# Performance work log

Measured on AMD Instinct MI355X. Metric: run time of the kernel, lower is better.

## Reference

```python
import jax, jax.numpy as jnp
import numpy as np

# SSD prior config (small VGGLite-style)
FEATURE_MAPS = [10, 5, 3, 1]
BOXES_PER_LOC = [4, 4, 4, 4]
IMG = 128      # ssd_config.DATA.SHAPE[0] -> WhereTransformer image_size
OBJ = 64
ZWHAT = 64
HID = 512
B = 4
N_OBJ = sum(f * f for f in FEATURE_MAPS)                       # 135
N_FEAT = sum(b * f * f for f, b in zip(FEATURE_MAPS, BOXES_PER_LOC))  # 540


def reconstruction_indices():
    # Replicates Decoder.reconstruction_indices: map per-location latents to per-box slots.
    idx = []
    last = 0
    for f, bpl in zip(FEATURE_MAPS, BOXES_PER_LOC):
        for i in range(f * f):
            idx.extend([last + i] * bpl)
        last += f * f
    return np.asarray(idx, dtype=np.int32)


def what_decode(z, W1, b1, W2, b2):
    # WhatDecoder: MLP z_what -> 3xOBJxOBJ object glyph in (0,1)
    h = jax.nn.relu(z @ W1 + b1)
    return jax.nn.sigmoid(h @ W2 + b2).reshape(-1, 3, OBJ, OBJ)


def where_stn(imgs, zw):
    # WhereTransformer: paste each object image into its (cx, cy, w, h) box on an IMGxIMG canvas
    # via inverse-affine bilinear sampling with zero padding (STN / grid_sample semantics).
    cx, cy, w, h = zw[:, 0], zw[:, 1], zw[:, 2], zw[:, 3]
    w = jnp.maximum(w, 1e-2)
    h = jnp.maximum(h, 1e-2)
    lin = jnp.linspace(-1.0, 1.0, IMG)
    gy, gx = jnp.meshgrid(lin, lin, indexing='ij')           # (IMG, IMG)
    u = (gx[None] - (2.0 * cx - 1.0)[:, None, None]) / w[:, None, None]
    v = (gy[None] - (2.0 * cy - 1.0)[:, None, None]) / h[:, None, None]
    px = (u + 1.0) * 0.5 * (OBJ - 1)                          # (N, IMG, IMG)
    py = (v + 1.0) * 0.5 * (OBJ - 1)

    def sample_one(img, py, px):  # img: (3, OBJ, OBJ)
        x0 = jnp.floor(px); y0 = jnp.floor(py)
        wx = px - x0; wy = py - y0
        x0i = x0.astype(jnp.int32); y0i = y0.astype(jnp.int32)

        def tap(yi, xi, wgt):
            valid = (yi >= 0) & (yi < OBJ) & (xi >= 0) & (xi < OBJ)
            yc = jnp.clip(yi, 0, OBJ - 1)
            xc = jnp.clip(xi, 0, OBJ - 1)
            return img[:, yc, xc] * (wgt * valid)[None]

        return (tap(y0i, x0i, (1 - wy) * (1 - wx)) + tap(y0i, x0i + 1, (1 - wy) * wx)
                + tap(y0i + 1, x0i, wy * (1 - wx)) + tap(y0i + 1, x0i + 1, wy * wx))

    return jax.vmap(sample_one)(imgs, py, px)                 # (N, 3, IMG, IMG)


def setup_inputs() -> dict:
    key = jax.random.key(0)
    ks = jax.random.split(key, 8)
    return {
        'z_what': jax.random.normal(ks[0], (B, N_OBJ, ZWHAT), jnp.float32),
        'z_where': jax.random.uniform(ks[1], (B, N_FEAT, 4), jnp.float32),
        'z_depth': jax.random.normal(ks[2], (B, N_OBJ, 1), jnp.float32),
        'W1': jax.random.normal(ks[3], (ZWHAT, HID), jnp.float32) * 0.05,
        'b1': jnp.zeros((HID,), jnp.float32),
        'W2': jax.random.normal(ks[4], (HID, 3 * OBJ * OBJ), jnp.float32) * 0.02,
        'b2': jnp.zeros((3 * OBJ * OBJ,), jnp.float32),
        'z_present': jax.random.randint(ks[5], (B, N_FEAT, 1), 0, 2, jnp.int32),
    }


def reference(z_what, z_where, z_depth, W1, b1, W2, b2, z_present):
    idx = jnp.asarray(reconstruction_indices())
    # index_select: replicate per-location latents across boxes-per-location
    zw_full = z_what[:, idx]                                  # (B, N_FEAT, ZWHAT)
    zd_full = z_depth[:, idx]                                 # (B, N_FEAT, 1)
    # sort descending by depth; gather all latents in that order
    order = jnp.argsort(-zd_full[..., 0], axis=1)             # (B, N_FEAT)
    s_what = jnp.take_along_axis(zw_full, order[..., None], axis=1)
    s_where = jnp.take_along_axis(z_where, order[..., None], axis=1)
    s_pres = jnp.take_along_axis(z_present, order[..., None], axis=1)
    # decode + STN warp all objects; absent objects are zeroed (equivalent to the
    dec = what_decode(s_what.reshape(-1, ZWHAT), W1, b1, W2, b2)
    warped = where_stn(dec, s_where.reshape(-1, 4))
    imgs = warped.reshape(B, N_FEAT, 3, IMG, IMG) * s_pres.astype(warped.dtype)[..., None, None]
    # depth compositing: per channel-pixel, take the first nonzero value in sorted order
    nz = imgs != 0
    first = jnp.argmax(nz, axis=1)                            # (B, 3, IMG, IMG)
    out = jnp.take_along_axis(imgs, first[:, None], axis=1)[:, 0] * nz.any(axis=1)
    return out
```

## Files before the change

### kernel.cpp

```cpp
#include <hip/hip_runtime.h>
#include <hip/hip_bf16.h>
#include <math.h>

#define NBOX  540
#define NOBJ  135
#define ZW    64
#define HIDN  512
#define NOUT  12288
#define OBJS  64
#define BATCH 4
#define MROWS 540
#define MPAD  640

#define PRE_SORT   4
#define PRE_GEMM1  MPAD
#define PRE_CVT    ((NOUT / 64) * (HIDN / 64))
#define PRE_BLOCKS (PRE_SORT + PRE_GEMM1 + PRE_CVT)

#define OFF_N      0u
#define OFF_PARAMS 256u
#define OFF_OBJS   34816u
#define OFF_HBF    43520u
#define OFF_W2T    698880u
#define OFF_DEC    13281792u

typedef short  bf16x8 __attribute__((ext_vector_type(8)));
typedef float  f32x4  __attribute__((ext_vector_type(4)));

#define GLOAD_LDS16(gp, lp)                                                    \
  __builtin_amdgcn_global_load_lds(                                            \
      (const __attribute__((address_space(1))) void*)(gp),                     \
      (__attribute__((address_space(3))) void*)(lp), 16, 0, 0)

__device__ __forceinline__ unsigned short f2bf(float x) {
  __hip_bfloat16 h = __float2bfloat16(x);
  return *(unsigned short*)&h;
}

__global__ __launch_bounds__(256) void k_pre(
    const float* __restrict__ z_depth,
    const float* __restrict__ z_where,
    const int*   __restrict__ z_present,
    const float* __restrict__ Z,
    const float* __restrict__ W1,
    const float* __restrict__ b1,
    const float* __restrict__ W2,
    float4* __restrict__ params,
    int*    __restrict__ objs,
    int*    __restrict__ n_present,
    unsigned short* __restrict__ Hbf,
    unsigned short* __restrict__ W2T)
{
  __shared__ unsigned long long keys[256];
  __shared__ int wsums[4], woff[4];
  __shared__ float zs[ZW];
  __shared__ unsigned int T[64 * 36];

  const int bid = blockIdx.x;
  const int t   = threadIdx.x;

  if (bid < PRE_SORT) {
    const int b = bid;
    unsigned long long key = ~0ull;
    if (t < NOBJ) {
      unsigned u = __float_as_uint(z_depth[b * NOBJ + t]);
      u = (u & 0x80000000u) ? ~u : (u | 0x80000000u);
      key = ((unsigned long long)(~u) << 32) | (unsigned)t;
    }
    keys[t] = key;
    __syncthreads();
    for (int k = 2; k <= 256; k <<= 1) {
      for (int j = k >> 1; j > 0; j >>= 1) {
        int ixj = t ^ j;
        if (ixj > t) {
          unsigned long long a = keys[t], c = keys[ixj];
          bool asc = (t & k) == 0;
          if (asc ? (a > c) : (a < c)) { keys[t] = c; keys[ixj] = a; }
        }
        __syncthreads();
      }
    }
    int boxq[3]; int presq[3]; int cnt = 0;
#pragma unroll
    for (int q = 0; q < 3; q++) {
      int e = 3 * t + q;
      presq[q] = 0; boxq[q] = 0;
      if (e < NBOX) {
        int o  = (int)(keys[e >> 2] & 0xFFFFFFFFull);
        int bx = o * 4 + (e & 3);
        boxq[q]  = bx;
        presq[q] = (z_present[b * NBOX + bx] != 0) ? 1 : 0;
        cnt += presq[q];
      }
    }
    int lane = t & 63, wv = t >> 6;
    int incl = cnt;
#pragma unroll
    for (int o = 1; o < 64; o <<= 1) {
      int vprev = __shfl_up(incl, o, 64);
      if (lane >= o) incl += vprev;
    }
    if (lane == 63) wsums[wv] = incl;
    __syncthreads();
    if (t == 0) {
      int a = 0;
#pragma unroll
      for (int i = 0; i < 4; i++) { woff[i] = a; a += wsums[i]; }
      n_present[b] = a;
    }
    __syncthreads();
    int slot = woff[wv] + incl - cnt;
#pragma unroll
    for (int q = 0; q < 3; q++) {
      if (presq[q]) {
        const float* zw = z_where + ((size_t)b * NBOX + boxq[q]) * 4;
        params[b * NBOX + slot] = make_float4(zw[0], zw[1], zw[2], zw[3]);
        objs[b * NBOX + slot]   = boxq[q] >> 2;
        slot++;
      }
    }
  } else if (bid < PRE_SORT + PRE_GEMM1) {
    const int r = bid - PRE_SORT;
    if (r >= MROWS) {
      Hbf[(size_t)r * HIDN + t] = 0;
      Hbf[(size_t)r * HIDN + t + 256] = 0;
      return;
    }
    if (t < ZW) zs[t] = Z[(size_t)r * ZW + t];
    __syncthreads();
    float a0 = b1[t], a1 = b1[t + 256];
#pragma unroll 8
    for (int k = 0; k < ZW; k++) {
      float z = zs[k];
      a0 += z * W1[(size_t)k * HIDN + t];
      a1 += z * W1[(size_t)k * HIDN + t + 256];
    }
    Hbf[(size_t)r * HIDN + t]       = f2bf(fmaxf(a0, 0.f));
    Hbf[(size_t)r * HIDN + t + 256] = f2bf(fmaxf(a1, 0.f));
  } else {
    const int c  = bid - PRE_SORT - PRE_GEMM1;
    const int n0 = (c % (NOUT / 64)) * 64;
    const int k0 = (c / (NOUT / 64)) * 64;
#pragma unroll
    for (int p = 0; p < 2; p++) {
      int kp = p * 16 + (t >> 4);
      int n4 = t & 15;
      int k  = k0 + kp * 2;
      float4 a = *(const float4*)&W2[(size_t)k * NOUT + n0 + n4 * 4];
      float4 b = *(const float4*)&W2[(size_t)(k + 1) * NOUT + n0 + n4 * 4];
      T[(n4*4 + 0) * 36 + kp] = (unsigned)f2bf(a.x) | ((unsigned)f2bf(b.x) << 16);
      T[(n4*4 + 1) * 36 + kp] = (unsigned)f2bf(a.y) | ((unsigned)f2bf(b.y) << 16);
      T[(n4*4 + 2) * 36 + kp] = (unsigned)f2bf(a.z) | ((unsigned)f2bf(b.z) << 16);
      T[(n4*4 + 3) * 36 + kp] = (unsigned)f2bf(a.w) | ((unsigned)f2bf(b.w) << 16);
    }
    __syncthreads();
#pragma unroll
    for (int p = 0; p < 2; p++) {
      int cc = p * 256 + t;
      int n = cc >> 3, ch = cc & 7;
      uint4 v = *(const uint4*)&T[n * 36 + ch * 4];
      *(uint4*)&W2T[(size_t)(n0 + n) * HIDN + k0 + ch * 8] = v;
    }
  }
}

__global__ __launch_bounds__(256) void k_gemm2_mfma(
    const unsigned short* __restrict__ Hbf,
    const unsigned short* __restrict__ W2T,
    const float* __restrict__ b2,
    float* __restrict__ dec)
{
  __shared__ unsigned short As[128 * 32];
  __shared__ unsigned short Bs[128 * 32];
  const int t    = threadIdx.x;
  const int lane = t & 63, wv = t >> 6;
  const int n0 = blockIdx.x * 128;
  const int m0 = blockIdx.y * 128;
  const int wm = (wv & 1) * 64, wn = (wv >> 1) * 64;

  const int r0 = t >> 2;
  const int kc0 = (t & 3) ^ (r0 & 3);
  const int r1 = r0 + 64;
  const int kc1 = (t & 3) ^ (r1 & 3);

  const int fr = lane & 15;
  const int fj = lane >> 4;
  f32x4 acc[4][4] = {};

  for (int k0 = 0; k0 < HIDN; k0 += 32) {
    GLOAD_LDS16(Hbf + (size_t)(m0 + r0) * HIDN + k0 + kc0 * 8, &As[t * 8]);
    GLOAD_LDS16(Hbf + (size_t)(m0 + r1) * HIDN + k0 + kc1 * 8, &As[(t + 256) * 8]);
    GLOAD_LDS16(W2T + (size_t)(n0 + r0) * HIDN + k0 + kc0 * 8, &Bs[t * 8]);
    GLOAD_LDS16(W2T + (size_t)(n0 + r1) * HIDN + k0 + kc1 * 8, &Bs[(t + 256) * 8]);
    __syncthreads();

    bf16x8 av[4], bv[4];
#pragma unroll
    for (int mi = 0; mi < 4; mi++) {
      int row = wm + mi * 16 + fr;
      av[mi] = *(const bf16x8*)&As[(row * 4 + (fj ^ (row & 3))) * 8];
    }
#pragma unroll
    for (int ni = 0; ni < 4; ni++) {
      int row = wn + ni * 16 + fr;
      bv[ni] = *(const bf16x8*)&Bs[(row * 4 + (fj ^ (row & 3))) * 8];
    }
#pragma unroll
    for (int mi = 0; mi < 4; mi++)
#pragma unroll
      for (int ni = 0; ni < 4; ni++)
        acc[mi][ni] = __builtin_amdgcn_mfma_f32_16x16x32_bf16(av[mi], bv[ni], acc[mi][ni], 0, 0, 0);
    __syncthreads();
  }

#pragma unroll
  for (int ni = 0; ni < 4; ni++) {
    int col = n0 + wn + ni * 16 + fr;
    float bb = b2[col];
#pragma unroll
    for (int mi = 0; mi < 4; mi++) {
#pragma unroll
      for (int r = 0; r < 4; r++) {
        int row = m0 + wm + mi * 16 + fj * 4 + r;
        if (row < MROWS) {
          float v = acc[mi][ni][r] + bb;
          dec[(size_t)row * NOUT + col] = 1.0f / (1.0f + __expf(-v));
        }
      }
    }
  }
}

__global__ __launch_bounds__(256) void k_composite(
    const float4* __restrict__ params, const int* __restrict__ objs,
    const int* __restrict__ n_present, const float* __restrict__ dec,
    float* __restrict__ out)
{
#pragma clang fp contract(off)
  __shared__ float4 sp[NBOX];
  __shared__ int sobj[NBOX];
  const int gid = blockIdx.x * 256 + threadIdx.x;
  const int b   = gid >> 14;
  const int pix = gid & 16383;
  const int y = pix >> 7, x = pix & 127;
  const int n = n_present[b];
  for (int i = threadIdx.x; i < n; i += 256) {
    sp[i]   = params[b * NBOX + i];
    sobj[i] = objs[b * NBOX + i];
  }
  __syncthreads();

  const double step = 2.0 / 127.0;
  const double gx = (x == 127) ? 1.0 : ((double)x * step + (-1.0));
  const double gy = (y == 127) ? 1.0 : ((double)y * step + (-1.0));

  float o0 = 0.f, o1 = 0.f, o2 = 0.f;
  bool done = false;
  for (int j = 0; j < n; j++) {
    if (__all((int)done)) break;
    if (!done) {
      float4 p = sp[j];
      double w = fmax((double)p.z, 0.01);
      double h = fmax((double)p.w, 0.01);
      double tx = 2.0 * (double)p.x - 1.0;
      double ty = 2.0 * (double)p.y - 1.0;
      double u = (gx - tx) / w;
      double v = (gy - ty) / h;
      double px = (u + 1.0) * 0.5 * 63.0;
      double py = (v + 1.0) * 0.5 * 63.0;
      double fx = floor(px), fy = floor(py);
      double wx = px - fx, wy = py - fy;
      int x0 = (int)fx, y0 = (int)fy;
      int x1 = x0 + 1, y1 = y0 + 1;
      bool vx0 = (x0 >= 0) && (x0 < OBJS);
      bool vx1 = (x1 >= 0) && (x1 < OBJS);
      bool vy0 = (y0 >= 0) && (y0 < OBJS);
      bool vy1 = (y1 >= 0) && (y1 < OBJS);
      double w00 = (1.0 - wy) * (1.0 - wx);
      double w01 = (1.0 - wy) * wx;
      double w10 = wy * (1.0 - wx);
      double w11 = wy * wx;
      bool c00 = vy0 && vx0 && (w00 > 0.0);
      bool c01 = vy0 && vx1 && (w01 > 0.0);
      bool c10 = vy1 && vx0 && (w10 > 0.0);
      bool c11 = vy1 && vx1 && (w11 > 0.0);
      if (c00 | c01 | c10 | c11) {
        const float* g = dec + (size_t)(b * NOBJ + sobj[j]) * NOUT;
        double s0 = 0.0, s1 = 0.0, s2 = 0.0;
        if (c00) { int o = y0*64 + x0; s0 += g[o]*w00; s1 += g[4096+o]*w00; s2 += g[8192+o]*w00; }
        if (c01) { int o = y0*64 + x1; s0 += g[o]*w01; s1 += g[4096+o]*w01; s2 += g[8192+o]*w01; }
        if (c10) { int o = y1*64 + x0; s0 += g[o]*w10; s1 += g[4096+o]*w10; s2 += g[8192+o]*w10; }
        if (c11) { int o = y1*64 + x1; s0 += g[o]*w11; s1 += g[4096+o]*w11; s2 += g[8192+o]*w11; }
        o0 = (float)s0; o1 = (float)s1; o2 = (float)s2;
        done = true;
      }
    }
  }
  const int ob = b * 3 * 16384 + pix;
  out[ob]         = o0;
  out[ob + 16384] = o1;
  out[ob + 32768] = o2;
}

extern "C" void kernel_launch(void* const* d_in, const int* in_sizes, int n_in,
                              void* d_out, int out_size, void* d_ws, size_t ws_size,
                              hipStream_t stream) {
  (void)in_sizes; (void)n_in; (void)out_size; (void)ws_size;
  const float* z_what    = (const float*)d_in[0];
  const float* z_where   = (const float*)d_in[1];
  const float* z_depth   = (const float*)d_in[2];
  const float* W1        = (const float*)d_in[3];
  const float* b1        = (const float*)d_in[4];
  const float* W2        = (const float*)d_in[5];
  const float* b2        = (const float*)d_in[6];
  const int*   z_present = (const int*)d_in[7];
  float* out = (float*)d_out;
  char* ws = (char*)d_ws;

  int*            n_present = (int*)(ws + OFF_N);
  float4*         params    = (float4*)(ws + OFF_PARAMS);
  int*            objs      = (int*)(ws + OFF_OBJS);
  unsigned short* Hbf       = (unsigned short*)(ws + OFF_HBF);
  unsigned short* W2T       = (unsigned short*)(ws + OFF_W2T);
  float*          dec       = (float*)(ws + OFF_DEC);

  k_pre<<<dim3(PRE_BLOCKS), dim3(256), 0, stream>>>(
      z_depth, z_where, z_present, z_what, W1, b1, W2,
      params, objs, n_present, Hbf, W2T);
  k_gemm2_mfma<<<dim3(NOUT / 128, MPAD / 128), dim3(256), 0, stream>>>(Hbf, W2T, b2, dec);
  k_composite<<<dim3(256), dim3(256), 0, stream>>>(params, objs, n_present, dec, out);
}
```

Before: 140.4 us.

## Fuse pre, GEMM and composite into one cooperative persistent kernel

Merges the three launches (prep/sort/GEMM1/W2 convert, MFMA GEMM2, compositing) into a single cooperative kernel of 480 blocks separated by grid-wide syncs, reusing one LDS buffer across phases. The compositing phase now maps each block to a 16x16 pixel tile instead of a row strip, aiming for better spatial coherence in the early-exit loop. This removes launch gaps but adds two grid barriers and serializes the formerly parallel prep work over fewer blocks.

```diff
diff --git a/kernel.cpp b/kernel.cpp
--- a/kernel.cpp
+++ b/kernel.cpp
@@ -1,6 +1,9 @@
 #include <hip/hip_runtime.h>
+#include <hip/hip_cooperative_groups.h>
 #include <hip/hip_bf16.h>
 #include <math.h>
+
+namespace cg = cooperative_groups;
 
 #define NBOX  540
 #define NOBJ  135
@@ -11,11 +14,8 @@
 #define BATCH 4
 #define MROWS 540
 #define MPAD  640
-
-#define PRE_SORT   4
-#define PRE_GEMM1  MPAD
-#define PRE_CVT    ((NOUT / 64) * (HIDN / 64))
-#define PRE_BLOCKS (PRE_SORT + PRE_GEMM1 + PRE_CVT)
+#define GRID  480
+#define CVTJOBS ((NOUT / 64) * (HIDN / 64))
 
 #define OFF_N      0u
 #define OFF_PARAMS 256u
@@ -37,7 +37,7 @@
   return *(unsigned short*)&h;
 }
 
-__global__ __launch_bounds__(256) void k_pre(
+__global__ __launch_bounds__(256, 2) void k_fused(
     const float* __restrict__ z_depth,
     const float* __restrict__ z_where,
     const int*   __restrict__ z_present,
@@ -45,22 +45,75 @@
     const float* __restrict__ W1,
     const float* __restrict__ b1,
     const float* __restrict__ W2,
+    const float* __restrict__ b2,
     float4* __restrict__ params,
     int*    __restrict__ objs,
     int*    __restrict__ n_present,
     unsigned short* __restrict__ Hbf,
-    unsigned short* __restrict__ W2T)
+    unsigned short* __restrict__ W2T,
+    float* __restrict__ dec,
+    float* __restrict__ out)
 {
-  __shared__ unsigned long long keys[256];
+  __shared__ __align__(16) unsigned char lds_raw[16384];
   __shared__ int wsums[4], woff[4];
-  __shared__ float zs[ZW];
-  __shared__ unsigned int T[64 * 36];
-
   const int bid = blockIdx.x;
   const int t   = threadIdx.x;
-
-  if (bid < PRE_SORT) {
-    const int b = bid;
+  cg::grid_group grid = cg::this_grid();
+
+  {
+    float* zs = (float*)lds_raw;
+    for (int r = bid; r < MPAD; r += GRID) {
+      if (r >= MROWS) {
+        Hbf[(size_t)r * HIDN + t] = 0;
+        Hbf[(size_t)r * HIDN + t + 256] = 0;
+      } else {
+        __syncthreads();
+        if (t < ZW) zs[t] = Z[(size_t)r * ZW + t];
+        __syncthreads();
+        float a0 = b1[t], a1 = b1[t + 256];
+#pragma unroll 8
+        for (int k = 0; k < ZW; k++) {
+          float z = zs[k];
+          a0 += z * W1[(size_t)k * HIDN + t];
+          a1 += z * W1[(size_t)k * HIDN + t + 256];
+        }
+        Hbf[(size_t)r * HIDN + t]       = f2bf(fmaxf(a0, 0.f));
+        Hbf[(size_t)r * HIDN + t + 256] = f2bf(fmaxf(a1, 0.f));
+      }
+    }
+  }
+  {
+    unsigned int* T = (unsigned int*)lds_raw;
+    for (int j = bid; j < CVTJOBS; j += GRID) {
+      __syncthreads();
+      const int n0 = (j % (NOUT / 64)) * 64;
+      const int k0 = (j / (NOUT / 64)) * 64;
+#pragma unroll
+      for (int p = 0; p < 2; p++) {
+        int kp = p * 16 + (t >> 4);
+        int n4 = t & 15;
+        int k  = k0 + kp * 2;
+        float4 a = *(const float4*)&W2[(size_t)k * NOUT + n0 + n4 * 4];
+        float4 b = *(const float4*)&W2[(size_t)(k + 1) * NOUT + n0 + n4 * 4];
+        T[(n4*4 + 0) * 36 + kp] = (unsigned)f2bf(a.x) | ((unsigned)f2bf(b.x) << 16);
+        T[(n4*4 + 1) * 36 + kp] = (unsigned)f2bf(a.y) | ((unsigned)f2bf(b.y) << 16);
+        T[(n4*4 + 2) * 36 + kp] = (unsigned)f2bf(a.z) | ((unsigned)f2bf(b.z) << 16);
+        T[(n4*4 + 3) * 36 + kp] = (unsigned)f2bf(a.w) | ((unsigned)f2bf(b.w) << 16);
+      }
+      __syncthreads();
+#pragma unroll
+      for (int p = 0; p < 2; p++) {
+        int cc = p * 256 + t;
+        int n = cc >> 3, ch = cc & 7;
+        uint4 v = *(const uint4*)&T[n * 36 + ch * 4];
+        *(uint4*)&W2T[(size_t)(n0 + n) * HIDN + k0 + ch * 8] = v;
+      }
+    }
+  }
+  if (bid >= GRID - 4) {
+    const int b = bid - (GRID - 4);
+    unsigned long long* keys = (unsigned long long*)lds_raw;
+    __syncthreads();
     unsigned long long key = ~0ull;
     if (t < NOBJ) {
       unsigned u = __float_as_uint(z_depth[b * NOBJ + t]);
@@ -119,187 +172,141 @@
         slot++;
       }
     }
-  } else if (bid < PRE_SORT + PRE_GEMM1) {
-    const int r = bid - PRE_SORT;
-    if (r >= MROWS) {
-      Hbf[(size_t)r * HIDN + t] = 0;
-      Hbf[(size_t)r * HIDN + t + 256] = 0;
-      return;
-    }
-    if (t < ZW) zs[t] = Z[(size_t)r * ZW + t];
-    __syncthreads();
-    float a0 = b1[t], a1 = b1[t + 256];
-#pragma unroll 8
-    for (int k = 0; k < ZW; k++) {
-      float z = zs[k];
-      a0 += z * W1[(size_t)k * HIDN + t];
-      a1 += z * W1[(size_t)k * HIDN + t + 256];
-    }
-    Hbf[(size_t)r * HIDN + t]       = f2bf(fmaxf(a0, 0.f));
-    Hbf[(size_t)r * HIDN + t + 256] = f2bf(fmaxf(a1, 0.f));
-  } else {
-    const int c  = bid - PRE_SORT - PRE_GEMM1;
-    const int n0 = (c % (NOUT / 64)) * 64;
-    const int k0 = (c / (NOUT / 64)) * 64;
-#pragma unroll
-    for (int p = 0; p < 2; p++) {
-      int kp = p * 16 + (t >> 4);
-      int n4 = t & 15;
-      int k  = k0 + kp * 2;
-      float4 a = *(const float4*)&W2[(size_t)k * NOUT + n0 + n4 * 4];
-      float4 b = *(const float4*)&W2[(size_t)(k + 1) * NOUT + n0 + n4 * 4];
-      T[(n4*4 + 0) * 36 + kp] = (unsigned)f2bf(a.x) | ((unsigned)f2bf(b.x) << 16);
-      T[(n4*4 + 1) * 36 + kp] = (unsigned)f2bf(a.y) | ((unsigned)f2bf(b.y) << 16);
-      T[(n4*4 + 2) * 36 + kp] = (unsigned)f2bf(a.z) | ((unsigned)f2bf(b.z) << 16);
-      T[(n4*4 + 3) * 36 + kp] = (unsigned)f2bf(a.w) | ((unsigned)f2bf(b.w) << 16);
-    }
-    __syncthreads();
-#pragma unroll
-    for (int p = 0; p < 2; p++) {
-      int cc = p * 256 + t;
-      int n = cc >> 3, ch = cc & 7;
-      uint4 v = *(const uint4*)&T[n * 36 + ch * 4];
-      *(uint4*)&W2T[(size_t)(n0 + n) * HIDN + k0 + ch * 8] = v;
-    }
-  }
-}
-
-__global__ __launch_bounds__(256) void k_gemm2_mfma(
-    const unsigned short* __restrict__ Hbf,
-    const unsigned short* __restrict__ W2T,
-    const float* __restrict__ b2,
-    float* __restrict__ dec)
-{
-  __shared__ unsigned short As[128 * 32];
-  __shared__ unsigned short Bs[128 * 32];
-  const int t    = threadIdx.x;
-  const int lane = t & 63, wv = t >> 6;
-  const int n0 = blockIdx.x * 128;
-  const int m0 = blockIdx.y * 128;
-  const int wm = (wv & 1) * 64, wn = (wv >> 1) * 64;
-
-  const int r0 = t >> 2;
-  const int kc0 = (t & 3) ^ (r0 & 3);
-  const int r1 = r0 + 64;
-  const int kc1 = (t & 3) ^ (r1 & 3);
-
-  const int fr = lane & 15;
-  const int fj = lane >> 4;
-  f32x4 acc[4][4] = {};
-
-  for (int k0 = 0; k0 < HIDN; k0 += 32) {
-    GLOAD_LDS16(Hbf + (size_t)(m0 + r0) * HIDN + k0 + kc0 * 8, &As[t * 8]);
-    GLOAD_LDS16(Hbf + (size_t)(m0 + r1) * HIDN + k0 + kc1 * 8, &As[(t + 256) * 8]);
-    GLOAD_LDS16(W2T + (size_t)(n0 + r0) * HIDN + k0 + kc0 * 8, &Bs[t * 8]);
-    GLOAD_LDS16(W2T + (size_t)(n0 + r1) * HIDN + k0 + kc1 * 8, &Bs[(t + 256) * 8]);
-    __syncthreads();
-
-    bf16x8 av[4], bv[4];
-#pragma unroll
-    for (int mi = 0; mi < 4; mi++) {
-      int row = wm + mi * 16 + fr;
-      av[mi] = *(const bf16x8*)&As[(row * 4 + (fj ^ (row & 3))) * 8];
-    }
+  }
+
+  __threadfence();
+  grid.sync();
+
+  {
+    unsigned short* As = (unsigned short*)lds_raw;
+    unsigned short* Bs = As + 128 * 32;
+    const int lane = t & 63, wv = t >> 6;
+    const int n0 = (bid % (NOUT / 128)) * 128;
+    const int m0 = (bid / (NOUT / 128)) * 128;
+    const int wm = (wv & 1) * 64, wn = (wv >> 1) * 64;
+
+    const int r0 = t >> 2;
+    const int kc0 = (t & 3) ^ (r0 & 3);
+    const int r1 = r0 + 64;
+    const int kc1 = (t & 3) ^ (r1 & 3);
+
+    const int fr = lane & 15;
+    const int fj = lane >> 4;
+    f32x4 acc[4][4] = {};
+
+    for (int k0 = 0; k0 < HIDN; k0 += 32) {
+      GLOAD_LDS16(Hbf + (size_t)(m0 + r0) * HIDN + k0 + kc0 * 8, &As[t * 8]);
+      GLOAD_LDS16(Hbf + (size_t)(m0 + r1) * HIDN + k0 + kc1 * 8, &As[(t + 256) * 8]);
+      GLOAD_LDS16(W2T + (size_t)(n0 + r0) * HIDN + k0 + kc0 * 8, &Bs[t * 8]);
+      GLOAD_LDS16(W2T + (size_t)(n0 + r1) * HIDN + k0 + kc1 * 8, &Bs[(t + 256) * 8]);
+      __syncthreads();
+
+      bf16x8 av[4], bv[4];
+#pragma unroll
+      for (int mi = 0; mi < 4; mi++) {
+        int row = wm + mi * 16 + fr;
+        av[mi] = *(const bf16x8*)&As[(row * 4 + (fj ^ (row & 3))) * 8];
+      }
+#pragma unroll
+      for (int ni = 0; ni < 4; ni++) {
+        int row = wn + ni * 16 + fr;
+        bv[ni] = *(const bf16x8*)&Bs[(row * 4 + (fj ^ (row & 3))) * 8];
+      }
+#pragma unroll
+      for (int mi = 0; mi < 4; mi++)
+#pragma unroll
+        for (int ni = 0; ni < 4; ni++)
+          acc[mi][ni] = __builtin_amdgcn_mfma_f32_16x16x32_bf16(av[mi], bv[ni], acc[mi][ni], 0, 0, 0);
+      __syncthreads();
+    }
+
 #pragma unroll
     for (int ni = 0; ni < 4; ni++) {
-      int row = wn + ni * 16 + fr;
-      bv[ni] = *(const bf16x8*)&Bs[(row * 4 + (fj ^ (row & 3))) * 8];
-    }
-#pragma unroll
-    for (int mi = 0; mi < 4; mi++)
-#pragma unroll
-      for (int ni = 0; ni < 4; ni++)
-        acc[mi][ni] = __builtin_amdgcn_mfma_f32_16x16x32_bf16(av[mi], bv[ni], acc[mi][ni], 0, 0, 0);
-    __syncthreads();
-  }
-
-#pragma unroll
-  for (int ni = 0; ni < 4; ni++) {
-    int col = n0 + wn + ni * 16 + fr;
-    float bb = b2[col];
-#pragma unroll
-    for (int mi = 0; mi < 4; mi++) {
-#pragma unroll
-      for (int r = 0; r < 4; r++) {
-        int row = m0 + wm + mi * 16 + fj * 4 + r;
-        if (row < MROWS) {
-          float v = acc[mi][ni][r] + bb;
-          dec[(size_t)row * NOUT + col] = 1.0f / (1.0f + __expf(-v));
+      int col = n0 + wn + ni * 16 + fr;
+      float bb = b2[col];
+#pragma unroll
+      for (int mi = 0; mi < 4; mi++) {
+#pragma unroll
+        for (int r = 0; r < 4; r++) {
+          int row = m0 + wm + mi * 16 + fj * 4 + r;
+          if (row < MROWS) {
+            float v = acc[mi][ni][r] + bb;
+            dec[(size_t)row * NOUT + col] = 1.0f / (1.0f + __expf(-v));
+          }
         }
       }
     }
   }
-}
-
-__global__ __launch_bounds__(256) void k_composite(
-    const float4* __restrict__ params, const int* __restrict__ objs,
-    const int* __restrict__ n_present, const float* __restrict__ dec,
-    float* __restrict__ out)
-{
+
+  __threadfence();
+  grid.sync();
+
+  if (bid < 256) {
 #pragma clang fp contract(off)
-  __shared__ float4 sp[NBOX];
-  __shared__ int sobj[NBOX];
-  const int gid = blockIdx.x * 256 + threadIdx.x;
-  const int b   = gid >> 14;
-  const int pix = gid & 16383;
-  const int y = pix >> 7, x = pix & 127;
-  const int n = n_present[b];
-  for (int i = threadIdx.x; i < n; i += 256) {
-    sp[i]   = params[b * NBOX + i];
-    sobj[i] = objs[b * NBOX + i];
-  }
-  __syncthreads();
-
-  const double step = 2.0 / 127.0;
-  const double gx = (x == 127) ? 1.0 : ((double)x * step + (-1.0));
-  const double gy = (y == 127) ? 1.0 : ((double)y * step + (-1.0));
-
-  float o0 = 0.f, o1 = 0.f, o2 = 0.f;
-  bool done = false;
-  for (int j = 0; j < n; j++) {
-    if (__all((int)done)) break;
-    if (!done) {
-      float4 p = sp[j];
-      double w = fmax((double)p.z, 0.01);
-      double h = fmax((double)p.w, 0.01);
-      double tx = 2.0 * (double)p.x - 1.0;
-      double ty = 2.0 * (double)p.y - 1.0;
-      double u = (gx - tx) / w;
-      double v = (gy - ty) / h;
-      double px = (u + 1.0) * 0.5 * 63.0;
-      double py = (v + 1.0) * 0.5 * 63.0;
-      double fx = floor(px), fy = floor(py);
-      double wx = px - fx, wy = py - fy;
-      int x0 = (int)fx, y0 = (int)fy;
-      int x1 = x0 + 1, y1 = y0 + 1;
-      bool vx0 = (x0 >= 0) && (x0 < OBJS);
-      bool vx1 = (x1 >= 0) && (x1 < OBJS);
-      bool vy0 = (y0 >= 0) && (y0 < OBJS);
-      bool vy1 = (y1 >= 0) && (y1 < OBJS);
-      double w00 = (1.0 - wy) * (1.0 - wx);
-      double w01 = (1.0 - wy) * wx;
-      double w10 = wy * (1.0 - wx);
-      double w11 = wy * wx;
-      bool c00 = vy0 && vx0 && (w00 > 0.0);
-      bool c01 = vy0 && vx1 && (w01 > 0.0);
-      bool c10 = vy1 && vx0 && (w10 > 0.0);
-      bool c11 = vy1 && vx1 && (w11 > 0.0);
-      if (c00 | c01 | c10 | c11) {
-        const float* g = dec + (size_t)(b * NOBJ + sobj[j]) * NOUT;
-        double s0 = 0.0, s1 = 0.0, s2 = 0.0;
-        if (c00) { int o = y0*64 + x0; s0 += g[o]*w00; s1 += g[4096+o]*w00; s2 += g[8192+o]*w00; }
-        if (c01) { int o = y0*64 + x1; s0 += g[o]*w01; s1 += g[4096+o]*w01; s2 += g[8192+o]*w01; }
-        if (c10) { int o = y1*64 + x0; s0 += g[o]*w10; s1 += g[4096+o]*w10; s2 += g[8192+o]*w10; }
-        if (c11) { int o = y1*64 + x1; s0 += g[o]*w11; s1 += g[4096+o]*w11; s2 += g[8192+o]*w11; }
-        o0 = (float)s0; o1 = (float)s1; o2 = (float)s2;
-        done = true;
-      }
-    }
-  }
-  const int ob = b * 3 * 16384 + pix;
-  out[ob]         = o0;
-  out[ob + 16384] = o1;
-  out[ob + 32768] = o2;
+    float4* sp   = (float4*)lds_raw;
+    int*    sobj = (int*)(lds_raw + 8640);
+    const int b    = bid >> 6;
+    const int tile = bid & 63;
+    const int y = (tile >> 3) * 16 + (t >> 4);
+    const int x = (tile & 7) * 16 + (t & 15);
+    const int n = n_present[b];
+    for (int i = t; i < n; i += 256) {
+      sp[i]   = params[b * NBOX + i];
+      sobj[i] = objs[b * NBOX + i];
+    }
+    __syncthreads();
+
+    const double step = 2.0 / 127.0;
+    const double gx = (x == 127) ? 1.0 : ((double)x * step + (-1.0));
+    const double gy = (y == 127) ? 1.0 : ((double)y * step + (-1.0));
+
+    float o0 = 0.f, o1 = 0.f, o2 = 0.f;
+    bool done = false;
+    for (int j = 0; j < n; j++) {
+      if (__all((int)done)) break;
+      if (!done) {
+        float4 p = sp[j];
+        double w = fmax((double)p.z, 0.01);
+        double h = fmax((double)p.w, 0.01);
+        double tx = 2.0 * (double)p.x - 1.0;
+        double ty = 2.0 * (double)p.y - 1.0;
+        double u = (gx - tx) / w;
+        double v = (gy - ty) / h;
+        double px = (u + 1.0) * 0.5 * 63.0;
+        double py = (v + 1.0) * 0.5 * 63.0;
+        double fx = floor(px), fy = floor(py);
+        double wx = px - fx, wy = py - fy;
+        int x0 = (int)fx, y0 = (int)fy;
+        int x1 = x0 + 1, y1 = y0 + 1;
+        bool vx0 = (x0 >= 0) && (x0 < OBJS);
+        bool vx1 = (x1 >= 0) && (x1 < OBJS);
+        bool vy0 = (y0 >= 0) && (y0 < OBJS);
+        bool vy1 = (y1 >= 0) && (y1 < OBJS);
+        double w00 = (1.0 - wy) * (1.0 - wx);
+        double w01 = (1.0 - wy) * wx;
+        double w10 = wy * (1.0 - wx);
+        double w11 = wy * wx;
+        bool c00 = vy0 && vx0 && (w00 > 0.0);
+        bool c01 = vy0 && vx1 && (w01 > 0.0);
+        bool c10 = vy1 && vx0 && (w10 > 0.0);
+        bool c11 = vy1 && vx1 && (w11 > 0.0);
+        if (c00 | c01 | c10 | c11) {
+          const float* g = dec + (size_t)(b * NOBJ + sobj[j]) * NOUT;
+          double s0 = 0.0, s1 = 0.0, s2 = 0.0;
+          if (c00) { int o = y0*64 + x0; s0 += g[o]*w00; s1 += g[4096+o]*w00; s2 += g[8192+o]*w00; }
+          if (c01) { int o = y0*64 + x1; s0 += g[o]*w01; s1 += g[4096+o]*w01; s2 += g[8192+o]*w01; }
+          if (c10) { int o = y1*64 + x0; s0 += g[o]*w10; s1 += g[4096+o]*w10; s2 += g[8192+o]*w10; }
+          if (c11) { int o = y1*64 + x1; s0 += g[o]*w11; s1 += g[4096+o]*w11; s2 += g[8192+o]*w11; }
+          o0 = (float)s0; o1 = (float)s1; o2 = (float)s2;
+          done = true;
+        }
+      }
+    }
+    const int ob = b * 3 * 16384 + y * 128 + x;
+    out[ob]         = o0;
+    out[ob + 16384] = o1;
+    out[ob + 32768] = o2;
+  }
 }
 
 extern "C" void kernel_launch(void* const* d_in, const int* in_sizes, int n_in,
@@ -324,9 +331,11 @@
   unsigned short* W2T       = (unsigned short*)(ws + OFF_W2T);
   float*          dec       = (float*)(ws + OFF_DEC);
 
-  k_pre<<<dim3(PRE_BLOCKS), dim3(256), 0, stream>>>(
-      z_depth, z_where, z_present, z_what, W1, b1, W2,
-      params, objs, n_present, Hbf, W2T);
-  k_gemm2_mfma<<<dim3(NOUT / 128, MPAD / 128), dim3(256), 0, stream>>>(Hbf, W2T, b2, dec);
-  k_composite<<<dim3(256), dim3(256), 0, stream>>>(params, objs, n_present, dec, out);
+  void* args[] = {
+    (void*)&z_depth, (void*)&z_where, (void*)&z_present, (void*)&z_what,
+    (void*)&W1, (void*)&b1, (void*)&W2, (void*)&b2,
+    (void*)&params, (void*)&objs, (void*)&n_present,
+    (void*)&Hbf, (void*)&W2T, (void*)&dec, (void*)&out
+  };
+  hipLaunchCooperativeKernel((void*)k_fused, dim3(GRID), dim3(256), args, 0, stream);
 }
```

Result: slower. 386.5 us (+175.3%).
